# Optimization experiments

Measured on AMD Instinct MI355X. Metric: run time of the kernel, lower is better.

The kernel has to match this reference:

```python
import jax, jax.numpy as jnp
import numpy as np

B, S, D, H, W = 8, 2048, 128, 8, 64
INT_HEADS = 8          # hardcoded in SpatioTemporalLayer1
EPS_COS = 1e-8
EPS_LN = 1e-5


def _mha(q_in, k_in, v_in, in_w, in_b, out_w, out_b, nh, mask=None):
    # q_in/k_in/v_in: (batch, len, d); torch nn.MultiheadAttention math (eval, no dropout)
    b, lq, d = q_in.shape
    hd = d // nh
    q = (q_in @ in_w[:d].T + in_b[:d]).reshape(b, lq, nh, hd)
    k = (k_in @ in_w[d:2 * d].T + in_b[d:2 * d]).reshape(b, k_in.shape[1], nh, hd)
    v = (v_in @ in_w[2 * d:].T + in_b[2 * d:]).reshape(b, v_in.shape[1], nh, hd)
    scores = jnp.einsum('bihd,bjhd->bhij', q, k) / jnp.sqrt(jnp.asarray(hd, q_in.dtype))
    if mask is not None:
        scores = scores + mask
    attn = jax.nn.softmax(scores, axis=-1)
    out = jnp.einsum('bhij,bjhd->bihd', attn, v).reshape(b, lq, d)
    return out @ out_w.T + out_b


def _layernorm(x, g, b):
    mu = x.mean(-1, keepdims=True)
    var = ((x - mu) ** 2).mean(-1, keepdims=True)
    return (x - mu) * jax.lax.rsqrt(var + EPS_LN) * g + b


def _cos_normalize(e):
    n = jnp.maximum(jnp.linalg.norm(e, axis=-1, keepdims=True), EPS_COS)
    return e / n


def _forward(x, spatial_info, temporal_info,
             lw_in_w, lw_in_b, lw_out_w, lw_out_b,
             spat_w, spat_b, temp_w, temp_b,
             int_in_w, int_in_b, int_out_w, int_out_b,
             ffn_w1, ffn_b1, ffn_w2, ffn_b2,
             ln1_g, ln1_b, ln2_g, ln2_b):
    b, s, d = x.shape
    # --- local window attention (S % W == 0 here, so no padding path) ---
    nw = s // W
    xw = x.reshape(b * nw, W, d)
    causal = jnp.triu(jnp.full((W, W), -jnp.inf, x.dtype), k=1)
    attn = _mha(xw, xw, xw, lw_in_w, lw_in_b, lw_out_w, lw_out_b, H, causal).reshape(b, s, d)
    x = _layernorm(attn + x, ln1_g, ln1_b)
    # --- FFN (torch nn.GELU default = exact erf) ---
    h = jax.nn.gelu(x @ ffn_w1.T + ffn_b1, approximate=False)
    x = _layernorm(h @ ffn_w2.T + ffn_b2 + x, ln2_g, ln2_b)
    # --- spatio-temporal interaction ---
    se = spatial_info @ spat_w.T + spat_b
    te = temporal_info @ temp_w.T + temp_b
    sn = _cos_normalize(se)
    tn = _cos_normalize(te)
    ss = jnp.einsum('bid,bjd->bij', sn, sn)   # (B,S,S) spatial cosine sim
    ts = jnp.einsum('bid,bjd->bij', tn, tn)   # (B,S,S) temporal cosine sim
    # interaction MHA is batch_first=False: it treats (B,S,D) as (len=B, batch=S, d).
    # Equivalent batch-first call on swapped axes (faithful to the torch source).
    inter = jnp.swapaxes(
        _mha(jnp.swapaxes(se, 0, 1), jnp.swapaxes(te, 0, 1), jnp.swapaxes(te, 0, 1),
             int_in_w, int_in_b, int_out_w, int_out_b, INT_HEADS), 0, 1)
    # similarity[b,i,j,d] = ss[b,i,j]*ts[b,i,j]*inter[b,i,d]; mean over j factorizes:
    sim = (ss * ts).mean(axis=2)              # (B,S)
    return x + sim[..., None] * inter


def setup_inputs() -> dict:
    key = jax.random.key(0)
    ks = jax.random.split(key, 24)
    sc = 0.02
    inp = {
        'x': jax.random.normal(ks[0], (B, S, D), jnp.float32),
        'spatial_info': jax.random.normal(ks[1], (B, S, D), jnp.float32),
        'temporal_info': jax.random.normal(ks[2], (B, S, D), jnp.float32),
        'lw_in_w': jax.random.normal(ks[3], (3 * D, D), jnp.float32) * sc,
        'lw_in_b': jnp.zeros((3 * D,), jnp.float32),
        'lw_out_w': jax.random.normal(ks[4], (D, D), jnp.float32) * sc,
        'lw_out_b': jnp.zeros((D,), jnp.float32),
        'spat_w': jax.random.normal(ks[5], (D, D), jnp.float32) * sc,
        'spat_b': jnp.zeros((D,), jnp.float32),
        'temp_w': jax.random.normal(ks[6], (D, D), jnp.float32) * sc,
        'temp_b': jnp.zeros((D,), jnp.float32),
        'int_in_w': jax.random.normal(ks[7], (3 * D, D), jnp.float32) * sc,
        'int_in_b': jnp.zeros((3 * D,), jnp.float32),
        'int_out_w': jax.random.normal(ks[8], (D, D), jnp.float32) * sc,
        'int_out_b': jnp.zeros((D,), jnp.float32),
        'ffn_w1': jax.random.normal(ks[9], (4 * D, D), jnp.float32) * sc,
        'ffn_b1': jnp.zeros((4 * D,), jnp.float32),
        'ffn_w2': jax.random.normal(ks[10], (D, 4 * D), jnp.float32) * sc,
        'ffn_b2': jnp.zeros((D,), jnp.float32),
        'ln1_g': jnp.ones((D,), jnp.float32),
        'ln1_b': jnp.zeros((D,), jnp.float32),
        'ln2_g': jnp.ones((D,), jnp.float32),
        'ln2_b': jnp.zeros((D,), jnp.float32),
    }
    return inp


def reference(x, spatial_info, temporal_info,
              lw_in_w, lw_in_b, lw_out_w, lw_out_b,
              spat_w, spat_b, temp_w, temp_b,
              int_in_w, int_in_b, int_out_w, int_out_b,
              ffn_w1, ffn_b1, ffn_w2, ffn_b2,
              ln1_g, ln1_b, ln2_g, ln2_b):
    return _forward(x, spatial_info, temporal_info,
                    lw_in_w, lw_in_b, lw_out_w, lw_out_b,
                    spat_w, spat_b, temp_w, temp_b,
                    int_in_w, int_in_b, int_out_w, int_out_b,
                    ffn_w1, ffn_b1, ffn_w2, ffn_b2,
                    ln1_g, ln1_b, ln2_g, ln2_b)
```

## Files before the change

kernel.cpp:

```cpp
#include <hip/hip_runtime.h>
#include <math.h>

#define BB 8
#define SS 2048
#define NTOK (BB * SS)

using bf16x8 = __attribute__((ext_vector_type(8))) short;
using f32x4  = __attribute__((ext_vector_type(4))) float;

__device__ __forceinline__ float gelu_tanh(float x) {
    float y = 0.7978845608f * (x + 0.044715f * x * x * x);
    float e = __expf(2.0f * y);
    float t = 1.0f - 2.0f / (e + 1.0f);
    return 0.5f * x * (1.0f + t);
}
__device__ __forceinline__ unsigned short f2b(float f) {
    unsigned int u = __float_as_uint(f);
    u += 0x7FFFu + ((u >> 16) & 1u);
    return (unsigned short)(u >> 16);
}
__device__ __forceinline__ float b2f(unsigned short u) {
    return __uint_as_float((unsigned int)u << 16);
}
__device__ __forceinline__ bf16x8 ldg_f32_b8(const float* p) {
    float4 f0 = *(const float4*)p, f1 = *(const float4*)(p + 4);
    union { ushort4 u[2]; bf16x8 v; } r;
    r.u[0] = (ushort4){f2b(f0.x), f2b(f0.y), f2b(f0.z), f2b(f0.w)};
    r.u[1] = (ushort4){f2b(f1.x), f2b(f1.y), f2b(f1.z), f2b(f1.w)};
    return r.v;
}

__global__ __launch_bounds__(256) void phase0(
    const float* __restrict__ x,
    const float* __restrict__ lw_in_w, const float* __restrict__ b_in,
    const float* __restrict__ lw_out_w,
    const float* __restrict__ spat_w, const float* __restrict__ temp_w,
    const float* __restrict__ ffn_w1, const float* __restrict__ ffn_w2,
    const float* __restrict__ int_in_w, const float* __restrict__ int_out_w,
    const float* __restrict__ spatial, const float* __restrict__ temporal,
    unsigned short* __restrict__ Wlwob, unsigned short* __restrict__ Wstb,
    unsigned short* __restrict__ Wb,
    unsigned short* __restrict__ Wib, unsigned short* __restrict__ Wiob,
    unsigned short* __restrict__ spb, unsigned short* __restrict__ tpb,
    unsigned short* __restrict__ qkvb,
    float* __restrict__ Mf)
{
    const int tid = threadIdx.x;
    if (blockIdx.x < 256) {
        const int m0 = blockIdx.x * 64;
        const int wv = tid >> 6, lane = tid & 63, ln = lane & 15, q = lane >> 4;
        const int wm = (wv >> 1) * 32, wn = (wv & 1) * 64;
        bf16x8 afr[4][2];
        #pragma unroll
        for (int kf = 0; kf < 4; ++kf)
            #pragma unroll
            for (int fm = 0; fm < 2; ++fm)
                afr[kf][fm] = ldg_f32_b8(x + (size_t)(m0 + wm + fm * 16 + ln) * 128 + kf * 32 + q * 8);
        #pragma unroll
        for (int p = 0; p < 3; ++p) {
            f32x4 acc[2][4] = {};
            #pragma unroll
            for (int kf = 0; kf < 4; ++kf) {
                bf16x8 b[4];
                #pragma unroll
                for (int fn = 0; fn < 4; ++fn)
                    b[fn] = ldg_f32_b8(lw_in_w + (size_t)(p * 128 + wn + fn * 16 + ln) * 128 + kf * 32 + q * 8);
                #pragma unroll
                for (int fm = 0; fm < 2; ++fm)
                    #pragma unroll
                    for (int fn = 0; fn < 4; ++fn)
                        acc[fm][fn] = __builtin_amdgcn_mfma_f32_16x16x32_bf16(afr[kf][fm], b[fn], acc[fm][fn], 0, 0, 0);
            }
            #pragma unroll
            for (int fm = 0; fm < 2; ++fm)
                #pragma unroll
                for (int r = 0; r < 4; ++r) {
                    int rl = wm + fm * 16 + q * 4 + r;
                    #pragma unroll
                    for (int fn = 0; fn < 4; ++fn) {
                        int col = wn + fn * 16 + ln;
                        qkvb[(size_t)(m0 + rl) * 384 + p * 128 + col] =
                            f2b(acc[fm][fn][r] + b_in[p * 128 + col]);
                    }
                }
        }
        return;
    }
    int v = (blockIdx.x - 256) * 256 + tid;
    if (v < 61440) {
        const float* src; unsigned short* dst; int off;
        if (v < 4096)       { src = lw_out_w;  dst = Wlwob;         off = v; }
        else if (v < 8192)  { src = spat_w;    dst = Wstb;          off = v - 4096; }
        else if (v < 12288) { src = temp_w;    dst = Wstb + 16384;  off = v - 8192; }
        else if (v < 28672) { src = ffn_w1;    dst = Wb;            off = v - 12288; }
        else if (v < 45056) { src = ffn_w2;    dst = Wb + 65536;    off = v - 28672; }
        else if (v < 57344) { src = int_in_w;  dst = Wib;           off = v - 45056; }
        else                { src = int_out_w; dst = Wiob;          off = v - 57344; }
        float4 f = *(const float4*)(src + (size_t)off * 4);
        *(ushort4*)(dst + (size_t)off * 4) =
            (ushort4){f2b(f.x), f2b(f.y), f2b(f.z), f2b(f.w)};
    } else if (v < 94208) {
        *(float4*)(Mf + (size_t)(v - 61440) * 4) = (float4){0.f, 0.f, 0.f, 0.f};
    } else {
        int u = v - 94208;
        const float* src; unsigned short* dst;
        if (u < 524288) { src = spatial;  dst = spb; }
        else            { src = temporal; dst = tpb; u -= 524288; }
        float4 f = *(const float4*)(src + (size_t)u * 4);
        *(ushort4*)(dst + (size_t)u * 4) =
            (ushort4){f2b(f.x), f2b(f.y), f2b(f.z), f2b(f.w)};
    }
}

__global__ __launch_bounds__(256) void phase1(
    const float* __restrict__ x,
    const unsigned short* __restrict__ qkvb,
    const unsigned short* __restrict__ lwoutb,
    const float* __restrict__ b_out,
    const float* __restrict__ lng, const float* __restrict__ lnb,
    float* __restrict__ x1, unsigned short* __restrict__ x1b,
    const unsigned short* __restrict__ spb, const unsigned short* __restrict__ tpb,
    const unsigned short* __restrict__ spwb, const unsigned short* __restrict__ tpwb,
    const float* __restrict__ bsp, const float* __restrict__ btp,
    unsigned short* __restrict__ snb, unsigned short* __restrict__ tnb,
    unsigned short* __restrict__ seb, unsigned short* __restrict__ teb)
{
    __shared__ unsigned short Qs[64 * 136];
    __shared__ unsigned short Ks[64 * 136];
    __shared__ unsigned short Vt[128 * 72];
    __shared__ unsigned short Pb[4][32 * 72];
    __shared__ float red[2][128][2];
    const int tid = threadIdx.x;
    const int wv = tid >> 6, lane = tid & 63, ln = lane & 15, q = lane >> 4;

    if (blockIdx.x >= 256) {
        const int idx2 = blockIdx.x - 256;
        const int y = idx2 >> 7;
        const int m0 = (idx2 & 127) * 128;
        const unsigned short* Ab = y ? tpb : spb;
        const unsigned short* Wfb = y ? tpwb : spwb;
        const float* bias = y ? btp : bsp;
        unsigned short* nb = y ? tnb : snb;
        unsigned short* raw = y ? teb : seb;
        const int wm = (wv >> 1) * 64, wn = (wv & 1) * 64;

        f32x4 acc[4][4] = {};
        #pragma unroll
        for (int kf = 0; kf < 4; ++kf) {
            bf16x8 a[4], b[4];
            #pragma unroll
            for (int fm = 0; fm < 4; ++fm)
                a[fm] = *(const bf16x8*)&Ab[(size_t)(m0 + wm + fm * 16 + ln) * 128 + kf * 32 + q * 8];
            #pragma unroll
            for (int fn = 0; fn < 4; ++fn)
                b[fn] = *(const bf16x8*)&Wfb[(size_t)(wn + fn * 16 + ln) * 128 + kf * 32 + q * 8];
            #pragma unroll
            for (int fm = 0; fm < 4; ++fm)
                #pragma unroll
                for (int fn = 0; fn < 4; ++fn)
                    acc[fm][fn] = __builtin_amdgcn_mfma_f32_16x16x32_bf16(a[fm], b[fn], acc[fm][fn], 0, 0, 0);
        }
        #pragma unroll
        for (int fm = 0; fm < 4; ++fm)
            #pragma unroll
            for (int r = 0; r < 4; ++r) {
                int rl = wm + fm * 16 + q * 4 + r;
                float s2 = 0.0f;
                #pragma unroll
                for (int fn = 0; fn < 4; ++fn) {
                    int col = wn + fn * 16 + ln;
                    float vv = acc[fm][fn][r] + bias[col];
                    acc[fm][fn][r] = vv;
                    s2 += vv * vv;
                }
                #pragma unroll
                for (int off = 1; off < 16; off <<= 1) s2 += __shfl_xor(s2, off, 64);
                if (ln == 0) red[0][rl][wv & 1] = s2;
            }
        __syncthreads();
        #pragma unroll
        for (int fm = 0; fm < 4; ++fm)
            #pragma unroll
            for (int r = 0; r < 4; ++r) {
                int rl = wm + fm * 16 + q * 4 + r;
                int row = m0 + rl;
                float inv = 1.0f / fmaxf(sqrtf(red[0][rl][0] + red[0][rl][1]), 1e-8f);
                #pragma unroll
                for (int fn = 0; fn < 4; ++fn) {
                    int col = wn + fn * 16 + ln;
                    float vv = acc[fm][fn][r];
                    nb[(size_t)row * 128 + col] = f2b(vv * inv);
                    raw[(size_t)row * 128 + col] = f2b(vv);
                }
            }
        return;
    }

    const int m0 = blockIdx.x * 64;
    const int wm = (wv >> 1) * 32, wn = (wv & 1) * 64;

    {
        const unsigned short* qrow = qkvb + (size_t)m0 * 384;
        #pragma unroll
        for (int t = 0; t < 12; ++t) {
            int idx = tid + t * 256;
            int r = idx / 48, c = (idx % 48) * 8;
            uint4 vv = *(const uint4*)&qrow[(size_t)r * 384 + c];
            if (c < 128)      *(uint4*)&Qs[r * 136 + c] = vv;
            else if (c < 256) *(uint4*)&Ks[r * 136 + (c - 128)] = vv;
            else {
                const unsigned short* pv = (const unsigned short*)&vv;
                #pragma unroll
                for (int c2 = 0; c2 < 8; ++c2)
                    Vt[(c - 256 + c2) * 72 + r] = pv[c2];
            }
        }
    }
    __syncthreads();

    {
        const int mh = wv >> 1, hq = wv & 1;
        unsigned short* P = &Pb[wv][0];
        #pragma unroll
        for (int hh = 0; hh < 4; ++hh) {
            const int h = hq * 4 + hh;
            f32x4 sacc[2][4] = {};
            bf16x8 az[2] = {}, bz[4] = {};
            if (q < 2) {
                #pragma unroll
                for (int fm = 0; fm < 2; ++fm)
                    az[fm] = *(const bf16x8*)&Qs[(mh * 32 + fm * 16 + ln) * 136 + h * 16 + q * 8];
                #pragma unroll
                for (int fn = 0; fn < 4; ++fn)
                    bz[fn] = *(const bf16x8*)&Ks[(fn * 16 + ln) * 136 + h * 16 + q * 8];
            }
            #pragma unroll
            for (int fm = 0; fm < 2; ++fm)
                #pragma unroll
                for (int fn = 0; fn < 4; ++fn)
                    sacc[fm][fn] = __builtin_amdgcn_mfma_f32_16x16x32_bf16(az[fm], bz[fn], sacc[fm][fn], 0, 0, 0);
            float invr[2][4];
            #pragma unroll
            for (int fm = 0; fm < 2; ++fm)
                #pragma unroll
                for (int r = 0; r < 4; ++r) {
                    int gi = mh * 32 + fm * 16 + q * 4 + r;
                    float mx = -1e30f;
                    #pragma unroll
                    for (int fn = 0; fn < 4; ++fn) {
                        int j = fn * 16 + ln;
                        float s = sacc[fm][fn][r] * 0.25f;
                        if (j > gi) s = -1e30f;
                        sacc[fm][fn][r] = s;
                        mx = fmaxf(mx, s);
                    }
                    #pragma unroll
                    for (int off = 1; off < 16; off <<= 1)
                        mx = fmaxf(mx, __shfl_xor(mx, off, 64));
                    float sum = 0.0f;
                    #pragma unroll
                    for (int fn = 0; fn < 4; ++fn) {
                        float p_ = __expf(sacc[fm][fn][r] - mx);
                        sacc[fm][fn][r] = p_;
                        sum += p_;
                    }
                    #pragma unroll
                    for (int off = 1; off < 16; off <<= 1)
                        sum += __shfl_xor(sum, off, 64);
                    invr[fm][r] = 1.0f / sum;
                    #pragma unroll
                    for (int fn = 0; fn < 4; ++fn)
                        P[(fm * 16 + q * 4 + r) * 72 + fn * 16 + ln] = f2b(sacc[fm][fn][r]);
                }
            f32x4 oacc[2] = {};
            #pragma unroll
            for (int kf2 = 0; kf2 < 2; ++kf2) {
                bf16x8 pa[2], vb;
                #pragma unroll
                for (int fm = 0; fm < 2; ++fm)
                    pa[fm] = *(const bf16x8*)&P[(fm * 16 + ln) * 72 + kf2 * 32 + q * 8];
                vb = *(const bf16x8*)&Vt[(h * 16 + ln) * 72 + kf2 * 32 + q * 8];
                #pragma unroll
                for (int fm = 0; fm < 2; ++fm)
                    oacc[fm] = __builtin_amdgcn_mfma_f32_16x16x32_bf16(pa[fm], vb, oacc[fm], 0, 0, 0);
            }
            #pragma unroll
            for (int fm = 0; fm < 2; ++fm)
                #pragma unroll
                for (int r = 0; r < 4; ++r)
                    Qs[(mh * 32 + fm * 16 + q * 4 + r) * 136 + h * 16 + ln] =
                        f2b(oacc[fm][r] * invr[fm][r]);
        }
    }
    __syncthreads();

    f32x4 acc[2][4] = {};
    #pragma unroll
    for (int kf = 0; kf < 4; ++kf) {
        bf16x8 a[2], b[4];
        #pragma unroll
        for (int fm = 0; fm < 2; ++fm)
            a[fm] = *(const bf16x8*)&Qs[(wm + fm * 16 + ln) * 136 + kf * 32 + q * 8];
        #pragma unroll
        for (int fn = 0; fn < 4; ++fn)
            b[fn] = *(const bf16x8*)&lwoutb[(size_t)(wn + fn * 16 + ln) * 128 + kf * 32 + q * 8];
        #pragma unroll
        for (int fm = 0; fm < 2; ++fm)
            #pragma unroll
            for (int fn = 0; fn < 4; ++fn)
                acc[fm][fn] = __builtin_amdgcn_mfma_f32_16x16x32_bf16(a[fm], b[fn], acc[fm][fn], 0, 0, 0);
    }
    #pragma unroll
    for (int fm = 0; fm < 2; ++fm)
        #pragma unroll
        for (int r = 0; r < 4; ++r) {
            int rl = wm + fm * 16 + q * 4 + r;
            int row = m0 + rl;
            float s1 = 0.0f, s2 = 0.0f;
            #pragma unroll
            for (int fn = 0; fn < 4; ++fn) {
                int col = wn + fn * 16 + ln;
                float vv = acc[fm][fn][r] + b_out[col] + x[(size_t)row * 128 + col];
                acc[fm][fn][r] = vv;
                s1 += vv; s2 += vv * vv;
            }
            #pragma unroll
            for (int off = 1; off < 16; off <<= 1) {
                s1 += __shfl_xor(s1, off, 64);
                s2 += __shfl_xor(s2, off, 64);
            }
            if (ln == 0) { red[0][rl][wv & 1] = s1; red[1][rl][wv & 1] = s2; }
        }
    __syncthreads();
    #pragma unroll
    for (int fm = 0; fm < 2; ++fm)
        #pragma unroll
        for (int r = 0; r < 4; ++r) {
            int rl = wm + fm * 16 + q * 4 + r;
            int row = m0 + rl;
            float mu = (red[0][rl][0] + red[0][rl][1]) * (1.0f / 128.0f);
            float var = (red[1][rl][0] + red[1][rl][1]) * (1.0f / 128.0f) - mu * mu;
            float rs = rsqrtf(var + 1e-5f);
            #pragma unroll
            for (int fn = 0; fn < 4; ++fn) {
                int col = wn + fn * 16 + ln;
                float o = (acc[fm][fn][r] - mu) * rs * lng[col] + lnb[col];
                x1[(size_t)row * 128 + col] = o;
                x1b[(size_t)row * 128 + col] = f2b(o);
            }
        }
}

__global__ __launch_bounds__(256) void ffn_kernel(
    const unsigned short* __restrict__ x1b, const float* __restrict__ x1,
    const unsigned short* __restrict__ Wb,
    const float* __restrict__ b1, const float* __restrict__ b2,
    const float* __restrict__ lng, const float* __restrict__ lnb,
    float* __restrict__ x2)
{
    __shared__ unsigned short Hw_s[4][16 * 72];
    __shared__ float part[3][16][132];
    const int tid = threadIdx.x;
    const int wv = tid >> 6, lane = tid & 63, ln = lane & 15, q = lane >> 4;
    const int t0 = blockIdx.x * 16;
    const int hh = wv;
    unsigned short* Hw = Hw_s[wv];
    const unsigned short* w1 = Wb;
    const unsigned short* w2 = Wb + 65536;

    bf16x8 afr[4];
    #pragma unroll
    for (int kf = 0; kf < 4; ++kf)
        afr[kf] = *(const bf16x8*)&x1b[(size_t)(t0 + ln) * 128 + kf * 32 + q * 8];

    f32x4 acc2[8] = {};
    #pragma unroll
    for (int ch = 0; ch < 2; ++ch) {
        const int hc0 = (hh * 2 + ch) * 64;
        f32x4 acc1[4] = {};
        #pragma unroll
        for (int kf = 0; kf < 4; ++kf) {
            bf16x8 b[4];
            #pragma unroll
            for (int fn = 0; fn < 4; ++fn)
                b[fn] = *(const bf16x8*)&w1[(size_t)(hc0 + fn * 16 + ln) * 128 + kf * 32 + q * 8];
            #pragma unroll
            for (int fn = 0; fn < 4; ++fn)
                acc1[fn] = __builtin_amdgcn_mfma_f32_16x16x32_bf16(afr[kf], b[fn], acc1[fn], 0, 0, 0);
        }
        #pragma unroll
        for (int fn = 0; fn < 4; ++fn)
            #pragma unroll
            for (int r = 0; r < 4; ++r)
                Hw[(q * 4 + r) * 72 + fn * 16 + ln] =
                    f2b(gelu_tanh(acc1[fn][r] + b1[hc0 + fn * 16 + ln]));
        #pragma unroll
        for (int kf2 = 0; kf2 < 2; ++kf2) {
            bf16x8 a = *(const bf16x8*)&Hw[ln * 72 + kf2 * 32 + q * 8];
            bf16x8 b8[8];
            #pragma unroll
            for (int fn = 0; fn < 8; ++fn)
                b8[fn] = *(const bf16x8*)&w2[(size_t)(fn * 16 + ln) * 512 + hc0 + kf2 * 32 + q * 8];
            #pragma unroll
            for (int fn = 0; fn < 8; ++fn)
                acc2[fn] = __builtin_amdgcn_mfma_f32_16x16x32_bf16(a, b8[fn], acc2[fn], 0, 0, 0);
        }
    }
    if (hh != 0) {
        #pragma unroll
        for (int fn = 0; fn < 8; ++fn)
            #pragma unroll
            for (int r = 0; r < 4; ++r)
                part[hh - 1][q * 4 + r][fn * 16 + ln] = acc2[fn][r];
    }
    __syncthreads();
    if (hh != 0) return;
    #pragma unroll
    for (int r = 0; r < 4; ++r) {
        int row = t0 + q * 4 + r;
        float s1 = 0.0f, s2 = 0.0f;
        #pragma unroll
        for (int fn = 0; fn < 8; ++fn) {
            int col = fn * 16 + ln;
            float vv = acc2[fn][r] + part[0][q * 4 + r][col] + part[1][q * 4 + r][col]
                     + part[2][q * 4 + r][col] + b2[col] + x1[(size_t)row * 128 + col];
            acc2[fn][r] = vv;
            s1 += vv; s2 += vv * vv;
        }
        #pragma unroll
        for (int off = 1; off < 16; off <<= 1) {
            s1 += __shfl_xor(s1, off, 64);
            s2 += __shfl_xor(s2, off, 64);
        }
        float mu = s1 * (1.0f / 128.0f);
        float var = s2 * (1.0f / 128.0f) - mu * mu;
        float rs = rsqrtf(var + 1e-5f);
        #pragma unroll
        for (int fn = 0; fn < 8; ++fn) {
            int col = fn * 16 + ln;
            x2[(size_t)row * 128 + col] = (acc2[fn][r] - mu) * rs * lng[col] + lnb[col];
        }
    }
}

__global__ __launch_bounds__(256) void atb_kernel(
    const unsigned short* __restrict__ snb, const unsigned short* __restrict__ tnb,
    float* __restrict__ Mf)
{
    __shared__ __align__(16) unsigned short Sst[64 * 136];
    __shared__ __align__(16) unsigned short Tst[64 * 136];
    const int tid = threadIdx.x;
    const int wv = tid >> 6, lane = tid & 63, ln = lane & 15, q = lane >> 4;
    const int idx2 = blockIdx.x;
    const int d0 = (idx2 & 1) * 64, e0 = ((idx2 >> 1) & 1) * 64;
    const int z = idx2 >> 2;
    const int b = z >> 4, chunk = z & 15;
    const size_t rowb = (size_t)(b * SS + chunk * 128);

    #pragma unroll
    for (int it = 0; it < 4; ++it) {
        int j = (tid & 31) + it * 32;
        int c8 = (tid >> 5) * 8;
        uint4 sv = *(const uint4*)&snb[(rowb + j) * 128 + d0 + c8];
        uint4 tv = *(const uint4*)&tnb[(rowb + j) * 128 + e0 + c8];
        const unsigned short* sp = (const unsigned short*)&sv;
        const unsigned short* tp = (const unsigned short*)&tv;
        #pragma unroll
        for (int c = 0; c < 8; ++c) {
            Sst[(c8 + c) * 136 + j] = sp[c];
            Tst[(c8 + c) * 136 + j] = tp[c];
        }
    }
    __syncthreads();

    const int wm = (wv >> 1) * 32, wn = (wv & 1) * 32;
    f32x4 acc[2][2] = {};
    #pragma unroll
    for (int kf = 0; kf < 4; ++kf) {
        bf16x8 a[2], bb[2];
        #pragma unroll
        for (int fm = 0; fm < 2; ++fm)
            a[fm] = *(const bf16x8*)&Tst[(wm + fm * 16 + ln) * 136 + kf * 32 + q * 8];
        #pragma unroll
        for (int fn = 0; fn < 2; ++fn)
            bb[fn] = *(const bf16x8*)&Sst[(wn + fn * 16 + ln) * 136 + kf * 32 + q * 8];
        #pragma unroll
        for (int fm = 0; fm < 2; ++fm)
            #pragma unroll
            for (int fn = 0; fn < 2; ++fn)
                acc[fm][fn] = __builtin_amdgcn_mfma_f32_16x16x32_bf16(a[fm], bb[fn], acc[fm][fn], 0, 0, 0);
    }
    float* pp = Mf + (size_t)b * 16384;
    #pragma unroll
    for (int fm = 0; fm < 2; ++fm)
        #pragma unroll
        for (int r = 0; r < 4; ++r) {
            int ee = e0 + wm + fm * 16 + q * 4 + r;
            #pragma unroll
            for (int fn = 0; fn < 2; ++fn) {
                int dd = d0 + wn + fn * 16 + ln;
                unsafeAtomicAdd(&pp[(size_t)ee * 128 + dd], acc[fm][fn][r]);
            }
        }
}

__global__ __launch_bounds__(256) void simgemm_kernel(
    const unsigned short* __restrict__ snb, const unsigned short* __restrict__ tnb,
    const float* __restrict__ Mf, float* __restrict__ sim)
{
    __shared__ float red[64][2];
    const int tid = threadIdx.x, m0 = blockIdx.x * 64, b = m0 >> 11;
    const int wv = tid >> 6, lane = tid & 63, ln = lane & 15, q = lane >> 4;
    const int wm = (wv >> 1) * 32, wn = (wv & 1) * 64;

    f32x4 acc[2][4] = {};
    #pragma unroll
    for (int kf = 0; kf < 4; ++kf) {
        bf16x8 a[2], bb[4];
        #pragma unroll
        for (int fm = 0; fm < 2; ++fm)
            a[fm] = *(const bf16x8*)&snb[(size_t)(m0 + wm + fm * 16 + ln) * 128 + kf * 32 + q * 8];
        #pragma unroll
        for (int fn = 0; fn < 4; ++fn)
            bb[fn] = ldg_f32_b8(Mf + (size_t)b * 16384 + (size_t)(wn + fn * 16 + ln) * 128 + kf * 32 + q * 8);
        #pragma unroll
        for (int fm = 0; fm < 2; ++fm)
            #pragma unroll
            for (int fn = 0; fn < 4; ++fn)
                acc[fm][fn] = __builtin_amdgcn_mfma_f32_16x16x32_bf16(a[fm], bb[fn], acc[fm][fn], 0, 0, 0);
    }
    #pragma unroll
    for (int fm = 0; fm < 2; ++fm)
        #pragma unroll
        for (int r = 0; r < 4; ++r) {
            int rl = wm + fm * 16 + q * 4 + r;
            int row = m0 + rl;
            float s = 0.0f;
            #pragma unroll
            for (int fn = 0; fn < 4; ++fn) {
                int col = wn + fn * 16 + ln;
                s += acc[fm][fn][r] * b2f(tnb[(size_t)row * 128 + col]);
            }
            #pragma unroll
            for (int off = 1; off < 16; off <<= 1) s += __shfl_xor(s, off, 64);
            if (ln == 0) red[rl][wv & 1] = s;
        }
    __syncthreads();
    if (tid < 64) sim[m0 + tid] = (red[tid][0] + red[tid][1]) * (1.0f / (float)SS);
}

__global__ __launch_bounds__(256) void inter_block(
    const unsigned short* __restrict__ seb, const unsigned short* __restrict__ teb,
    const unsigned short* __restrict__ Wib,
    const float* __restrict__ b_int,
    const unsigned short* __restrict__ Wiob,
    const float* __restrict__ b_io,
    const float* __restrict__ sim, const float* __restrict__ x2,
    float* __restrict__ out)
{
    __shared__ unsigned short Qs[64 * 136];
    __shared__ unsigned short KVs[64 * 256];
    const int tid = threadIdx.x, s0 = blockIdx.x * 8;
    const int wv = tid >> 6, lane = tid & 63, ln = lane & 15, q = lane >> 4;
    const int wm = (wv >> 1) * 32, wn = (wv & 1) * 64;

    bf16x8 afr[4][2];
    #pragma unroll
    for (int kf = 0; kf < 4; ++kf)
        #pragma unroll
        for (int fm = 0; fm < 2; ++fm) {
            int rl = wm + fm * 16 + ln;
            size_t g = (size_t)(rl >> 3) * 2048 + s0 + (rl & 7);
            afr[kf][fm] = *(const bf16x8*)&seb[g * 128 + kf * 32 + q * 8];
        }

    #pragma unroll
    for (int p = 0; p < 3; ++p) {
        if (p == 1) {
            #pragma unroll
            for (int kf = 0; kf < 4; ++kf)
                #pragma unroll
                for (int fm = 0; fm < 2; ++fm) {
                    int rl = wm + fm * 16 + ln;
                    size_t g = (size_t)(rl >> 3) * 2048 + s0 + (rl & 7);
                    afr[kf][fm] = *(const bf16x8*)&teb[g * 128 + kf * 32 + q * 8];
                }
        }
        f32x4 acc[2][4] = {};
        #pragma unroll
        for (int kf = 0; kf < 4; ++kf) {
            bf16x8 b[4];
            #pragma unroll
            for (int fn = 0; fn < 4; ++fn)
                b[fn] = *(const bf16x8*)&Wib[(size_t)(p * 128 + wn + fn * 16 + ln) * 128 + kf * 32 + q * 8];
            #pragma unroll
            for (int fm = 0; fm < 2; ++fm)
                #pragma unroll
                for (int fn = 0; fn < 4; ++fn)
                    acc[fm][fn] = __builtin_amdgcn_mfma_f32_16x16x32_bf16(afr[kf][fm], b[fn], acc[fm][fn], 0, 0, 0);
        }
        #pragma unroll
        for (int fm = 0; fm < 2; ++fm)
            #pragma unroll
            for (int r = 0; r < 4; ++r) {
                int rl = wm + fm * 16 + q * 4 + r;
                #pragma unroll
                for (int fn = 0; fn < 4; ++fn) {
                    int col = wn + fn * 16 + ln;
                    unsigned short v = f2b(acc[fm][fn][r] + b_int[p * 128 + col]);
                    if (p == 0) Qs[rl * 136 + col] = v;
                    else        KVs[rl * 256 + (p - 1) * 128 + col] = v;
                }
            }
        __syncthreads();
    }

    #pragma unroll
    for (int tt = 0; tt < 2; ++tt) {
        int task = tid + tt * 256;
        int ss = task >> 6, h = (task >> 3) & 7, i = task & 7;
        int rq = i * 8 + ss;
        float qr[16];
        {
            uint4 q0 = *(const uint4*)&Qs[rq * 136 + h * 16];
            uint4 q1 = *(const uint4*)&Qs[rq * 136 + h * 16 + 8];
            const unsigned short* p0 = (const unsigned short*)&q0;
            const unsigned short* p1 = (const unsigned short*)&q1;
            #pragma unroll
            for (int c = 0; c < 8; ++c) { qr[c] = b2f(p0[c]); qr[8 + c] = b2f(p1[c]); }
        }
        float sc[8];
        #pragma unroll
        for (int j = 0; j < 8; ++j) {
            uint4 k0 = *(const uint4*)&KVs[(j * 8 + ss) * 256 + h * 16];
            uint4 k1 = *(const uint4*)&KVs[(j * 8 + ss) * 256 + h * 16 + 8];
            const unsigned short* kp0 = (const unsigned short*)&k0;
            const unsigned short* kp1 = (const unsigned short*)&k1;
            float s = 0.0f;
            #pragma unroll
            for (int c = 0; c < 8; ++c) {
                s = fmaf(qr[c], b2f(kp0[c]), s);
                s = fmaf(qr[8 + c], b2f(kp1[c]), s);
            }
            sc[j] = s * 0.25f;
        }
        float mx = -1e30f;
        #pragma unroll
        for (int j = 0; j < 8; ++j) mx = fmaxf(mx, sc[j]);
        float pe[8], se = 0.0f;
        #pragma unroll
        for (int j = 0; j < 8; ++j) { pe[j] = __expf(sc[j] - mx); se += pe[j]; }
        float inv = 1.0f / se;
        float o[16] = {};
        #pragma unroll
        for (int j = 0; j < 8; ++j) {
            uint4 v0 = *(const uint4*)&KVs[(j * 8 + ss) * 256 + 128 + h * 16];
            uint4 v1 = *(const uint4*)&KVs[(j * 8 + ss) * 256 + 128 + h * 16 + 8];
            const unsigned short* vp0 = (const unsigned short*)&v0;
            const unsigned short* vp1 = (const unsigned short*)&v1;
            #pragma unroll
            for (int c = 0; c < 8; ++c) {
                o[c]     += pe[j] * b2f(vp0[c]);
                o[8 + c] += pe[j] * b2f(vp1[c]);
            }
        }
        ushort4 w0 = (ushort4){f2b(o[0]*inv),  f2b(o[1]*inv),  f2b(o[2]*inv),  f2b(o[3]*inv)};
        ushort4 w1 = (ushort4){f2b(o[4]*inv),  f2b(o[5]*inv),  f2b(o[6]*inv),  f2b(o[7]*inv)};
        ushort4 w2 = (ushort4){f2b(o[8]*inv),  f2b(o[9]*inv),  f2b(o[10]*inv), f2b(o[11]*inv)};
        ushort4 w3 = (ushort4){f2b(o[12]*inv), f2b(o[13]*inv), f2b(o[14]*inv), f2b(o[15]*inv)};
        *(ushort4*)&Qs[rq * 136 + h * 16]      = w0;
        *(ushort4*)&Qs[rq * 136 + h * 16 + 4]  = w1;
        *(ushort4*)&Qs[rq * 136 + h * 16 + 8]  = w2;
        *(ushort4*)&Qs[rq * 136 + h * 16 + 12] = w3;
    }
    __syncthreads();

    f32x4 acc[2][4] = {};
    #pragma unroll
    for (int kf = 0; kf < 4; ++kf) {
        bf16x8 a[2], b[4];
        #pragma unroll
        for (int fm = 0; fm < 2; ++fm)
            a[fm] = *(const bf16x8*)&Qs[(wm + fm * 16 + ln) * 136 + kf * 32 + q * 8];
        #pragma unroll
        for (int fn = 0; fn < 4; ++fn)
            b[fn] = *(const bf16x8*)&Wiob[(size_t)(wn + fn * 16 + ln) * 128 + kf * 32 + q * 8];
        #pragma unroll
        for (int fm = 0; fm < 2; ++fm)
            #pragma unroll
            for (int fn = 0; fn < 4; ++fn)
                acc[fm][fn] = __builtin_amdgcn_mfma_f32_16x16x32_bf16(a[fm], b[fn], acc[fm][fn], 0, 0, 0);
    }
    #pragma unroll
    for (int fm = 0; fm < 2; ++fm)
        #pragma unroll
        for (int r = 0; r < 4; ++r) {
            int rl = wm + fm * 16 + q * 4 + r;
            size_t g = (size_t)(rl >> 3) * 2048 + s0 + (rl & 7);
            float sc = sim[g];
            #pragma unroll
            for (int fn = 0; fn < 4; ++fn) {
                int col = wn + fn * 16 + ln;
                out[g * 128 + col] = (acc[fm][fn][r] + b_io[col]) * sc + x2[g * 128 + col];
            }
        }
}

extern "C" void kernel_launch(void* const* d_in, const int* in_sizes, int n_in,
                              void* d_out, int out_size, void* d_ws, size_t ws_size,
                              hipStream_t stream)
{
    const float* x        = (const float*)d_in[0];
    const float* spatial  = (const float*)d_in[1];
    const float* temporal = (const float*)d_in[2];
    const float* lw_in_w  = (const float*)d_in[3];
    const float* lw_in_b  = (const float*)d_in[4];
    const float* lw_out_w = (const float*)d_in[5];
    const float* lw_out_b = (const float*)d_in[6];
    const float* spat_w   = (const float*)d_in[7];
    const float* spat_b   = (const float*)d_in[8];
    const float* temp_w   = (const float*)d_in[9];
    const float* temp_b   = (const float*)d_in[10];
    const float* int_in_w = (const float*)d_in[11];
    const float* int_in_b = (const float*)d_in[12];
    const float* int_out_w= (const float*)d_in[13];
    const float* int_out_b= (const float*)d_in[14];
    const float* ffn_b1   = (const float*)d_in[16];
    const float* ffn_b2   = (const float*)d_in[18];
    const float* ln1_g    = (const float*)d_in[19];
    const float* ln1_b    = (const float*)d_in[20];
    const float* ln2_g    = (const float*)d_in[21];
    const float* ln2_b    = (const float*)d_in[22];
    float* out = (float*)d_out;

    char* base = (char*)d_ws;
    float*          x1    = (float*)(base + 0);
    unsigned short* x1b   = (unsigned short*)(base + 8388608);
    float*          x2    = (float*)(base + 12582912);
    unsigned short* snb   = (unsigned short*)(base + 20971520);
    unsigned short* tnb   = (unsigned short*)(base + 25165824);
    unsigned short* seb   = (unsigned short*)(base + 29360128);
    unsigned short* teb   = (unsigned short*)(base + 33554432);
    unsigned short* Wb    = (unsigned short*)(base + 37748736);
    unsigned short* Wib   = (unsigned short*)(base + 38010880);
    unsigned short* Wiob  = (unsigned short*)(base + 38109184);
    float*          simb  = (float*)(base + 38666240);
    unsigned short* Wlwob = (unsigned short*)(base + 38731776);
    unsigned short* Wstb  = (unsigned short*)(base + 38764544);
    unsigned short* spb   = (unsigned short*)(base + 38830080);
    unsigned short* tpb   = (unsigned short*)(base + 43024384);
    unsigned short* qkvb  = (unsigned short*)(base + 47218688);
    float*          Mf    = (float*)(base + 59801600);

    phase0<<<4720, 256, 0, stream>>>(
        x, lw_in_w, lw_in_b, lw_out_w, spat_w, temp_w,
        (const float*)d_in[15], (const float*)d_in[17], int_in_w, int_out_w,
        spatial, temporal,
        Wlwob, Wstb, Wb, Wib, Wiob, spb, tpb, qkvb, Mf);
    phase1<<<512, 256, 0, stream>>>(
        x, qkvb, Wlwob, lw_out_b, ln1_g, ln1_b, x1, x1b,
        spb, tpb, Wstb, Wstb + 16384, spat_b, temp_b,
        snb, tnb, seb, teb);
    ffn_kernel<<<1024, 256, 0, stream>>>(
        x1b, x1, Wb, ffn_b1, ffn_b2, ln2_g, ln2_b, x2);
    atb_kernel<<<512, 256, 0, stream>>>(snb, tnb, Mf);
    simgemm_kernel<<<256, 256, 0, stream>>>(snb, tnb, Mf, simb);
    inter_block<<<256, 256, 0, stream>>>(
        seb, teb, Wib, int_in_b, Wiob, int_out_b, simb, x2, out);
}
```

Measured before the change: 232.7 us.

## Fuse Tn^T·Sn reduction into projection blocks and merge FFN with sim GEMM

The spatial/temporal projection blocks in phase1 now compute both projections for a 64-row tile, stage the normalized tiles transposed in shared memory, and directly atomically accumulate the per-batch Tn^T·Sn matrix, removing the separate atb kernel and its reload of snb/tnb. The FFN kernel and the similarity GEMM are merged into a single launch with block-index dispatch, cutting two launches. This trades extra shared-memory reuse and more atomics per block (64-row chunks instead of 128) for fewer kernel launches and less global traffic.

```diff
diff --git a/kernel.cpp b/kernel.cpp
--- a/kernel.cpp
+++ b/kernel.cpp
@@ -123,7 +123,8 @@
     const unsigned short* __restrict__ spwb, const unsigned short* __restrict__ tpwb,
     const float* __restrict__ bsp, const float* __restrict__ btp,
     unsigned short* __restrict__ snb, unsigned short* __restrict__ tnb,
-    unsigned short* __restrict__ seb, unsigned short* __restrict__ teb)
+    unsigned short* __restrict__ seb, unsigned short* __restrict__ teb,
+    float* __restrict__ Mf)
 {
     __shared__ unsigned short Qs[64 * 136];
     __shared__ unsigned short Ks[64 * 136];
@@ -135,62 +136,108 @@
 
     if (blockIdx.x >= 256) {
         const int idx2 = blockIdx.x - 256;
-        const int y = idx2 >> 7;
-        const int m0 = (idx2 & 127) * 128;
-        const unsigned short* Ab = y ? tpb : spb;
-        const unsigned short* Wfb = y ? tpwb : spwb;
-        const float* bias = y ? btp : bsp;
-        unsigned short* nb = y ? tnb : snb;
-        unsigned short* raw = y ? teb : seb;
-        const int wm = (wv >> 1) * 64, wn = (wv & 1) * 64;
-
-        f32x4 acc[4][4] = {};
+        const int m0 = idx2 * 64;
+        const int b = m0 >> 11;
+        unsigned short* Snt = Vt;
+        unsigned short* Tnt = &Pb[0][0];
+        const int wm = (wv >> 1) * 32, wn = (wv & 1) * 64;
+
+        f32x4 acc0[2][4] = {}, acc1[2][4] = {};
         #pragma unroll
         for (int kf = 0; kf < 4; ++kf) {
-            bf16x8 a[4], b[4];
-            #pragma unroll
-            for (int fm = 0; fm < 4; ++fm)
-                a[fm] = *(const bf16x8*)&Ab[(size_t)(m0 + wm + fm * 16 + ln) * 128 + kf * 32 + q * 8];
-            #pragma unroll
-            for (int fn = 0; fn < 4; ++fn)
-                b[fn] = *(const bf16x8*)&Wfb[(size_t)(wn + fn * 16 + ln) * 128 + kf * 32 + q * 8];
-            #pragma unroll
-            for (int fm = 0; fm < 4; ++fm)
-                #pragma unroll
-                for (int fn = 0; fn < 4; ++fn)
-                    acc[fm][fn] = __builtin_amdgcn_mfma_f32_16x16x32_bf16(a[fm], b[fn], acc[fm][fn], 0, 0, 0);
-        }
-        #pragma unroll
-        for (int fm = 0; fm < 4; ++fm)
+            bf16x8 a0[2], a1[2], b0[4], b1[4];
+            #pragma unroll
+            for (int fm = 0; fm < 2; ++fm) {
+                a0[fm] = *(const bf16x8*)&spb[(size_t)(m0 + wm + fm * 16 + ln) * 128 + kf * 32 + q * 8];
+                a1[fm] = *(const bf16x8*)&tpb[(size_t)(m0 + wm + fm * 16 + ln) * 128 + kf * 32 + q * 8];
+            }
+            #pragma unroll
+            for (int fn = 0; fn < 4; ++fn) {
+                b0[fn] = *(const bf16x8*)&spwb[(size_t)(wn + fn * 16 + ln) * 128 + kf * 32 + q * 8];
+                b1[fn] = *(const bf16x8*)&tpwb[(size_t)(wn + fn * 16 + ln) * 128 + kf * 32 + q * 8];
+            }
+            #pragma unroll
+            for (int fm = 0; fm < 2; ++fm)
+                #pragma unroll
+                for (int fn = 0; fn < 4; ++fn) {
+                    acc0[fm][fn] = __builtin_amdgcn_mfma_f32_16x16x32_bf16(a0[fm], b0[fn], acc0[fm][fn], 0, 0, 0);
+                    acc1[fm][fn] = __builtin_amdgcn_mfma_f32_16x16x32_bf16(a1[fm], b1[fn], acc1[fm][fn], 0, 0, 0);
+                }
+        }
+        #pragma unroll
+        for (int fm = 0; fm < 2; ++fm)
             #pragma unroll
             for (int r = 0; r < 4; ++r) {
                 int rl = wm + fm * 16 + q * 4 + r;
-                float s2 = 0.0f;
+                float s20 = 0.0f, s21 = 0.0f;
                 #pragma unroll
                 for (int fn = 0; fn < 4; ++fn) {
                     int col = wn + fn * 16 + ln;
-                    float vv = acc[fm][fn][r] + bias[col];
-                    acc[fm][fn][r] = vv;
-                    s2 += vv * vv;
-                }
-                #pragma unroll
-                for (int off = 1; off < 16; off <<= 1) s2 += __shfl_xor(s2, off, 64);
-                if (ln == 0) red[0][rl][wv & 1] = s2;
+                    float v0 = acc0[fm][fn][r] + bsp[col];
+                    float v1 = acc1[fm][fn][r] + btp[col];
+                    acc0[fm][fn][r] = v0;
+                    acc1[fm][fn][r] = v1;
+                    s20 += v0 * v0; s21 += v1 * v1;
+                }
+                #pragma unroll
+                for (int off = 1; off < 16; off <<= 1) {
+                    s20 += __shfl_xor(s20, off, 64);
+                    s21 += __shfl_xor(s21, off, 64);
+                }
+                if (ln == 0) { red[0][rl][wv & 1] = s20; red[1][rl][wv & 1] = s21; }
             }
         __syncthreads();
         #pragma unroll
-        for (int fm = 0; fm < 4; ++fm)
+        for (int fm = 0; fm < 2; ++fm)
             #pragma unroll
             for (int r = 0; r < 4; ++r) {
                 int rl = wm + fm * 16 + q * 4 + r;
                 int row = m0 + rl;
-                float inv = 1.0f / fmaxf(sqrtf(red[0][rl][0] + red[0][rl][1]), 1e-8f);
+                float inv0 = 1.0f / fmaxf(sqrtf(red[0][rl][0] + red[0][rl][1]), 1e-8f);
+                float inv1 = 1.0f / fmaxf(sqrtf(red[1][rl][0] + red[1][rl][1]), 1e-8f);
                 #pragma unroll
                 for (int fn = 0; fn < 4; ++fn) {
                     int col = wn + fn * 16 + ln;
-                    float vv = acc[fm][fn][r];
-                    nb[(size_t)row * 128 + col] = f2b(vv * inv);
-                    raw[(size_t)row * 128 + col] = f2b(vv);
+                    float v0 = acc0[fm][fn][r];
+                    float v1 = acc1[fm][fn][r];
+                    unsigned short n0 = f2b(v0 * inv0);
+                    unsigned short n1 = f2b(v1 * inv1);
+                    snb[(size_t)row * 128 + col] = n0;
+                    seb[(size_t)row * 128 + col] = f2b(v0);
+                    tnb[(size_t)row * 128 + col] = n1;
+                    teb[(size_t)row * 128 + col] = f2b(v1);
+                    Snt[col * 72 + rl] = n0;
+                    Tnt[col * 72 + rl] = n1;
+                }
+            }
+        __syncthreads();
+        const int e0q = (wv >> 1) * 64, d0q = (wv & 1) * 64;
+        f32x4 macc[4][4] = {};
+        #pragma unroll
+        for (int kf2 = 0; kf2 < 2; ++kf2) {
+            bf16x8 a[4], bb[4];
+            #pragma unroll
+            for (int fm = 0; fm < 4; ++fm)
+                a[fm] = *(const bf16x8*)&Tnt[(e0q + fm * 16 + ln) * 72 + kf2 * 32 + q * 8];
+            #pragma unroll
+            for (int fn = 0; fn < 4; ++fn)
+                bb[fn] = *(const bf16x8*)&Snt[(d0q + fn * 16 + ln) * 72 + kf2 * 32 + q * 8];
+            #pragma unroll
+            for (int fm = 0; fm < 4; ++fm)
+                #pragma unroll
+                for (int fn = 0; fn < 4; ++fn)
+                    macc[fm][fn] = __builtin_amdgcn_mfma_f32_16x16x32_bf16(a[fm], bb[fn], macc[fm][fn], 0, 0, 0);
+        }
+        float* pp = Mf + (size_t)b * 16384;
+        #pragma unroll
+        for (int fm = 0; fm < 4; ++fm)
+            #pragma unroll
+            for (int r = 0; r < 4; ++r) {
+                int ee = e0q + fm * 16 + q * 4 + r;
+                #pragma unroll
+                for (int fn = 0; fn < 4; ++fn) {
+                    int dd = d0q + fn * 16 + ln;
+                    unsafeAtomicAdd(&pp[(size_t)ee * 128 + dd], macc[fm][fn][r]);
                 }
             }
         return;
@@ -351,202 +398,143 @@
         }
 }
 
-__global__ __launch_bounds__(256) void ffn_kernel(
+__global__ __launch_bounds__(256) void phase2(
     const unsigned short* __restrict__ x1b, const float* __restrict__ x1,
     const unsigned short* __restrict__ Wb,
     const float* __restrict__ b1, const float* __restrict__ b2,
     const float* __restrict__ lng, const float* __restrict__ lnb,
-    float* __restrict__ x2)
+    float* __restrict__ x2,
+    const unsigned short* __restrict__ snb, const unsigned short* __restrict__ tnb,
+    const float* __restrict__ Mf, float* __restrict__ sim)
 {
     __shared__ unsigned short Hw_s[4][16 * 72];
     __shared__ float part[3][16][132];
+    __shared__ float red[64][2];
     const int tid = threadIdx.x;
     const int wv = tid >> 6, lane = tid & 63, ln = lane & 15, q = lane >> 4;
-    const int t0 = blockIdx.x * 16;
-    const int hh = wv;
-    unsigned short* Hw = Hw_s[wv];
-    const unsigned short* w1 = Wb;
-    const unsigned short* w2 = Wb + 65536;
-
-    bf16x8 afr[4];
-    #pragma unroll
-    for (int kf = 0; kf < 4; ++kf)
-        afr[kf] = *(const bf16x8*)&x1b[(size_t)(t0 + ln) * 128 + kf * 32 + q * 8];
-
-    f32x4 acc2[8] = {};
-    #pragma unroll
-    for (int ch = 0; ch < 2; ++ch) {
-        const int hc0 = (hh * 2 + ch) * 64;
-        f32x4 acc1[4] = {};
+
+    if (blockIdx.x < 1024) {
+        const int t0 = blockIdx.x * 16;
+        const int hh = wv;
+        unsigned short* Hw = Hw_s[wv];
+        const unsigned short* w1 = Wb;
+        const unsigned short* w2 = Wb + 65536;
+
+        bf16x8 afr[4];
+        #pragma unroll
+        for (int kf = 0; kf < 4; ++kf)
+            afr[kf] = *(const bf16x8*)&x1b[(size_t)(t0 + ln) * 128 + kf * 32 + q * 8];
+
+        f32x4 acc2[8] = {};
+        #pragma unroll
+        for (int ch = 0; ch < 2; ++ch) {
+            const int hc0 = (hh * 2 + ch) * 64;
+            f32x4 acc1[4] = {};
+            #pragma unroll
+            for (int kf = 0; kf < 4; ++kf) {
+                bf16x8 b[4];
+                #pragma unroll
+                for (int fn = 0; fn < 4; ++fn)
+                    b[fn] = *(const bf16x8*)&w1[(size_t)(hc0 + fn * 16 + ln) * 128 + kf * 32 + q * 8];
+                #pragma unroll
+                for (int fn = 0; fn < 4; ++fn)
+                    acc1[fn] = __builtin_amdgcn_mfma_f32_16x16x32_bf16(afr[kf], b[fn], acc1[fn], 0, 0, 0);
+            }
+            #pragma unroll
+            for (int fn = 0; fn < 4; ++fn)
+                #pragma unroll
+                for (int r = 0; r < 4; ++r)
+                    Hw[(q * 4 + r) * 72 + fn * 16 + ln] =
+                        f2b(gelu_tanh(acc1[fn][r] + b1[hc0 + fn * 16 + ln]));
+            #pragma unroll
+            for (int kf2 = 0; kf2 < 2; ++kf2) {
+                bf16x8 a = *(const bf16x8*)&Hw[ln * 72 + kf2 * 32 + q * 8];
+                bf16x8 b8[8];
+                #pragma unroll
+                for (int fn = 0; fn < 8; ++fn)
+                    b8[fn] = *(const bf16x8*)&w2[(size_t)(fn * 16 + ln) * 512 + hc0 + kf2 * 32 + q * 8];
+                #pragma unroll
+                for (int fn = 0; fn < 8; ++fn)
+                    acc2[fn] = __builtin_amdgcn_mfma_f32_16x16x32_bf16(a, b8[fn], acc2[fn], 0, 0, 0);
+            }
+        }
+        if (hh != 0) {
+            #pragma unroll
+            for (int fn = 0; fn < 8; ++fn)
+                #pragma unroll
+                for (int r = 0; r < 4; ++r)
+                    part[hh - 1][q * 4 + r][fn * 16 + ln] = acc2[fn][r];
+        }
+        __syncthreads();
+        if (hh != 0) return;
+        #pragma unroll
+        for (int r = 0; r < 4; ++r) {
+            int row = t0 + q * 4 + r;
+            float s1 = 0.0f, s2 = 0.0f;
+            #pragma unroll
+            for (int fn = 0; fn < 8; ++fn) {
+                int col = fn * 16 + ln;
+                float vv = acc2[fn][r] + part[0][q * 4 + r][col] + part[1][q * 4 + r][col]
+                         + part[2][q * 4 + r][col] + b2[col] + x1[(size_t)row * 128 + col];
+                acc2[fn][r] = vv;
+                s1 += vv; s2 += vv * vv;
+            }
+            #pragma unroll
+            for (int off = 1; off < 16; off <<= 1) {
+                s1 += __shfl_xor(s1, off, 64);
+                s2 += __shfl_xor(s2, off, 64);
+            }
+            float mu = s1 * (1.0f / 128.0f);
+            float var = s2 * (1.0f / 128.0f) - mu * mu;
+            float rs = rsqrtf(var + 1e-5f);
+            #pragma unroll
+            for (int fn = 0; fn < 8; ++fn) {
+                int col = fn * 16 + ln;
+                x2[(size_t)row * 128 + col] = (acc2[fn][r] - mu) * rs * lng[col] + lnb[col];
+            }
+        }
+        return;
+    }
+
+    {
+        const int m0 = (blockIdx.x - 1024) * 64, b = m0 >> 11;
+        const int wm = (wv >> 1) * 32, wn = (wv & 1) * 64;
+
+        f32x4 acc[2][4] = {};
         #pragma unroll
         for (int kf = 0; kf < 4; ++kf) {
-            bf16x8 b[4];
+            bf16x8 a[2], bb[4];
+            #pragma unroll
+            for (int fm = 0; fm < 2; ++fm)
+                a[fm] = *(const bf16x8*)&snb[(size_t)(m0 + wm + fm * 16 + ln) * 128 + kf * 32 + q * 8];
             #pragma unroll
             for (int fn = 0; fn < 4; ++fn)
-                b[fn] = *(const bf16x8*)&w1[(size_t)(hc0 + fn * 16 + ln) * 128 + kf * 32 + q * 8];
-            #pragma unroll
-            for (int fn = 0; fn < 4; ++fn)
-                acc1[fn] = __builtin_amdgcn_mfma_f32_16x16x32_bf16(afr[kf], b[fn], acc1[fn], 0, 0, 0);
-        }
-        #pragma unroll
-        for (int fn = 0; fn < 4; ++fn)
-            #pragma unroll
-            for (int r = 0; r < 4; ++r)
-                Hw[(q * 4 + r) * 72 + fn * 16 + ln] =
-                    f2b(gelu_tanh(acc1[fn][r] + b1[hc0 + fn * 16 + ln]));
-        #pragma unroll
-        for (int kf2 = 0; kf2 < 2; ++kf2) {
-            bf16x8 a = *(const bf16x8*)&Hw[ln * 72 + kf2 * 32 + q * 8];
-            bf16x8 b8[8];
-            #pragma unroll
-            for (int fn = 0; fn < 8; ++fn)
-                b8[fn] = *(const bf16x8*)&w2[(size_t)(fn * 16 + ln) * 512 + hc0 + kf2 * 32 + q * 8];
-            #pragma unroll
-            for (int fn = 0; fn < 8; ++fn)
-                acc2[fn] = __builtin_amdgcn_mfma_f32_16x16x32_bf16(a, b8[fn], acc2[fn], 0, 0, 0);
-        }
-    }
-    if (hh != 0) {
-        #pragma unroll
-        for (int fn = 0; fn < 8; ++fn)
-            #pragma unroll
-            for (int r = 0; r < 4; ++r)
-                part[hh - 1][q * 4 + r][fn * 16 + ln] = acc2[fn][r];
-    }
-    __syncthreads();
-    if (hh != 0) return;
-    #pragma unroll
-    for (int r = 0; r < 4; ++r) {
-        int row = t0 + q * 4 + r;
-        float s1 = 0.0f, s2 = 0.0f;
-        #pragma unroll
-        for (int fn = 0; fn < 8; ++fn) {
-            int col = fn * 16 + ln;
-            float vv = acc2[fn][r] + part[0][q * 4 + r][col] + part[1][q * 4 + r][col]
-                     + part[2][q * 4 + r][col] + b2[col] + x1[(size_t)row * 128 + col];
-            acc2[fn][r] = vv;
-            s1 += vv; s2 += vv * vv;
-        }
-        #pragma unroll
-        for (int off = 1; off < 16; off <<= 1) {
-            s1 += __shfl_xor(s1, off, 64);
-            s2 += __shfl_xor(s2, off, 64);
-        }
-        float mu = s1 * (1.0f / 128.0f);
-        float var = s2 * (1.0f / 128.0f) - mu * mu;
-        float rs = rsqrtf(var + 1e-5f);
-        #pragma unroll
-        for (int fn = 0; fn < 8; ++fn) {
-            int col = fn * 16 + ln;
-            x2[(size_t)row * 128 + col] = (acc2[fn][r] - mu) * rs * lng[col] + lnb[col];
-        }
-    }
-}
-
-__global__ __launch_bounds__(256) void atb_kernel(
-    const unsigned short* __restrict__ snb, const unsigned short* __restrict__ tnb,
-    float* __restrict__ Mf)
-{
-    __shared__ __align__(16) unsigned short Sst[64 * 136];
-    __shared__ __align__(16) unsigned short Tst[64 * 136];
-    const int tid = threadIdx.x;
-    const int wv = tid >> 6, lane = tid & 63, ln = lane & 15, q = lane >> 4;
-    const int idx2 = blockIdx.x;
-    const int d0 = (idx2 & 1) * 64, e0 = ((idx2 >> 1) & 1) * 64;
-    const int z = idx2 >> 2;
-    const int b = z >> 4, chunk = z & 15;
-    const size_t rowb = (size_t)(b * SS + chunk * 128);
-
-    #pragma unroll
-    for (int it = 0; it < 4; ++it) {
-        int j = (tid & 31) + it * 32;
-        int c8 = (tid >> 5) * 8;
-        uint4 sv = *(const uint4*)&snb[(rowb + j) * 128 + d0 + c8];
-        uint4 tv = *(const uint4*)&tnb[(rowb + j) * 128 + e0 + c8];
-        const unsigned short* sp = (const unsigned short*)&sv;
-        const unsigned short* tp = (const unsigned short*)&tv;
-        #pragma unroll
-        for (int c = 0; c < 8; ++c) {
-            Sst[(c8 + c) * 136 + j] = sp[c];
-            Tst[(c8 + c) * 136 + j] = tp[c];
-        }
-    }
-    __syncthreads();
-
-    const int wm = (wv >> 1) * 32, wn = (wv & 1) * 32;
-    f32x4 acc[2][2] = {};
-    #pragma unroll
-    for (int kf = 0; kf < 4; ++kf) {
-        bf16x8 a[2], bb[2];
+                bb[fn] = ldg_f32_b8(Mf + (size_t)b * 16384 + (size_t)(wn + fn * 16 + ln) * 128 + kf * 32 + q * 8);
+            #pragma unroll
+            for (int fm = 0; fm < 2; ++fm)
+                #pragma unroll
+                for (int fn = 0; fn < 4; ++fn)
+                    acc[fm][fn] = __builtin_amdgcn_mfma_f32_16x16x32_bf16(a[fm], bb[fn], acc[fm][fn], 0, 0, 0);
+        }
         #pragma unroll
         for (int fm = 0; fm < 2; ++fm)
-            a[fm] = *(const bf16x8*)&Tst[(wm + fm * 16 + ln) * 136 + kf * 32 + q * 8];
-        #pragma unroll
-        for (int fn = 0; fn < 2; ++fn)
-            bb[fn] = *(const bf16x8*)&Sst[(wn + fn * 16 + ln) * 136 + kf * 32 + q * 8];
-        #pragma unroll
-        for (int fm = 0; fm < 2; ++fm)
-            #pragma unroll
-            for (int fn = 0; fn < 2; ++fn)
-                acc[fm][fn] = __builtin_amdgcn_mfma_f32_16x16x32_bf16(a[fm], bb[fn], acc[fm][fn], 0, 0, 0);
-    }
-    float* pp = Mf + (size_t)b * 16384;
-    #pragma unroll
-    for (int fm = 0; fm < 2; ++fm)
-        #pragma unroll
-        for (int r = 0; r < 4; ++r) {
-            int ee = e0 + wm + fm * 16 + q * 4 + r;
-            #pragma unroll
-            for (int fn = 0; fn < 2; ++fn) {
-                int dd = d0 + wn + fn * 16 + ln;
-                unsafeAtomicAdd(&pp[(size_t)ee * 128 + dd], acc[fm][fn][r]);
-            }
-        }
-}
-
-__global__ __launch_bounds__(256) void simgemm_kernel(
-    const unsigned short* __restrict__ snb, const unsigned short* __restrict__ tnb,
-    const float* __restrict__ Mf, float* __restrict__ sim)
-{
-    __shared__ float red[64][2];
-    const int tid = threadIdx.x, m0 = blockIdx.x * 64, b = m0 >> 11;
-    const int wv = tid >> 6, lane = tid & 63, ln = lane & 15, q = lane >> 4;
-    const int wm = (wv >> 1) * 32, wn = (wv & 1) * 64;
-
-    f32x4 acc[2][4] = {};
-    #pragma unroll
-    for (int kf = 0; kf < 4; ++kf) {
-        bf16x8 a[2], bb[4];
-        #pragma unroll
-        for (int fm = 0; fm < 2; ++fm)
-            a[fm] = *(const bf16x8*)&snb[(size_t)(m0 + wm + fm * 16 + ln) * 128 + kf * 32 + q * 8];
-        #pragma unroll
-        for (int fn = 0; fn < 4; ++fn)
-            bb[fn] = ldg_f32_b8(Mf + (size_t)b * 16384 + (size_t)(wn + fn * 16 + ln) * 128 + kf * 32 + q * 8);
-        #pragma unroll
-        for (int fm = 0; fm < 2; ++fm)
-            #pragma unroll
-            for (int fn = 0; fn < 4; ++fn)
-                acc[fm][fn] = __builtin_amdgcn_mfma_f32_16x16x32_bf16(a[fm], bb[fn], acc[fm][fn], 0, 0, 0);
-    }
-    #pragma unroll
-    for (int fm = 0; fm < 2; ++fm)
-        #pragma unroll
-        for (int r = 0; r < 4; ++r) {
-            int rl = wm + fm * 16 + q * 4 + r;
-            int row = m0 + rl;
-            float s = 0.0f;
-            #pragma unroll
-            for (int fn = 0; fn < 4; ++fn) {
-                int col = wn + fn * 16 + ln;
-                s += acc[fm][fn][r] * b2f(tnb[(size_t)row * 128 + col]);
-            }
-            #pragma unroll
-            for (int off = 1; off < 16; off <<= 1) s += __shfl_xor(s, off, 64);
-            if (ln == 0) red[rl][wv & 1] = s;
-        }
-    __syncthreads();
-    if (tid < 64) sim[m0 + tid] = (red[tid][0] + red[tid][1]) * (1.0f / (float)SS);
+            #pragma unroll
+            for (int r = 0; r < 4; ++r) {
+                int rl = wm + fm * 16 + q * 4 + r;
+                int row = m0 + rl;
+                float s = 0.0f;
+                #pragma unroll
+                for (int fn = 0; fn < 4; ++fn) {
+                    int col = wn + fn * 16 + ln;
+                    s += acc[fm][fn][r] * b2f(tnb[(size_t)row * 128 + col]);
+                }
+                #pragma unroll
+                for (int off = 1; off < 16; off <<= 1) s += __shfl_xor(s, off, 64);
+                if (ln == 0) red[rl][wv & 1] = s;
+            }
+        __syncthreads();
+        if (tid < 64) sim[m0 + tid] = (red[tid][0] + red[tid][1]) * (1.0f / (float)SS);
+    }
 }
 
 __global__ __launch_bounds__(256) void inter_block(
@@ -760,11 +748,9 @@
     phase1<<<512, 256, 0, stream>>>(
         x, qkvb, Wlwob, lw_out_b, ln1_g, ln1_b, x1, x1b,
         spb, tpb, Wstb, Wstb + 16384, spat_b, temp_b,
-        snb, tnb, seb, teb);
-    ffn_kernel<<<1024, 256, 0, stream>>>(
-        x1b, x1, Wb, ffn_b1, ffn_b2, ln2_g, ln2_b, x2);
-    atb_kernel<<<512, 256, 0, stream>>>(snb, tnb, Mf);
-    simgemm_kernel<<<256, 256, 0, stream>>>(snb, tnb, Mf, simb);
+        snb, tnb, seb, teb, Mf);
+    phase2<<<1280, 256, 0, stream>>>(
+        x1b, x1, Wb, ffn_b1, ffn_b2, ln2_g, ln2_b, x2, snb, tnb, Mf, simb);
     inter_block<<<256, 256, 0, stream>>>(
         seb, teb, Wib, int_in_b, Wiob, int_out_b, simb, x2, out);
 }
```

New measurement: 234.1 us. About the same (+0.6%).
